# Optimization experiments

Hardware: AMD Instinct MI355X
Metric: run time of the kernel (lower is better)

Reference implementation:

```python
import jax, jax.numpy as jnp
import numpy as np

N = 50000
E = 600000
D = 128
H = 8
DH = D // H
SCALE = float(np.sqrt(DH))


def setup_inputs() -> dict:
    key = jax.random.key(0)
    ks = jax.random.split(key, 12)
    s = 1.0 / np.sqrt(D)
    return {
        "x": jax.random.normal(ks[0], (N, D), jnp.float32),
        "edge_index": jax.random.randint(ks[1], (2, E), 0, N, jnp.int64),
        "edge_attr": jax.random.normal(ks[2], (E,), jnp.float32),
        "Wq": jax.random.uniform(ks[3], (D, D), jnp.float32, -s, s),
        "bq": jax.random.uniform(ks[4], (D,), jnp.float32, -s, s),
        "Wk": jax.random.uniform(ks[5], (D, D), jnp.float32, -s, s),
        "bk": jax.random.uniform(ks[6], (D,), jnp.float32, -s, s),
        "Wv": jax.random.uniform(ks[7], (D, D), jnp.float32, -s, s),
        "bv": jax.random.uniform(ks[8], (D,), jnp.float32, -s, s),
        "Wo": jax.random.uniform(ks[9], (D, D), jnp.float32, -s, s),
        "bo": jax.random.uniform(ks[10], (D,), jnp.float32, -s, s),
    }


def reference(x, edge_index, edge_attr, Wq, bq, Wk, bk, Wv, bv, Wo, bo):
    # Projections -> [N, H, DH]
    Q = (x @ Wq + bq).reshape(N, H, DH)
    K = (x @ Wk + bk).reshape(N, H, DH)
    V = (x @ Wv + bv).reshape(N, H, DH)
    row, col = edge_index[0], edge_index[1]
    q_i = Q[row]   # [E, H, DH] gather by destination (source of softmax segment)
    k_j = K[col]
    v_j = V[col]
    scores = jnp.sum(q_i * k_j, axis=-1) / SCALE  # [E, H]
    scores = scores + edge_attr[:, None]          # edge_attr broadcast over heads
    # Segment softmax per row-node; max is taken over heads then per node (as original)
    edge_max = scores.max(axis=1)                                  # [E]
    node_max = jax.ops.segment_max(edge_max, row, num_segments=N)  # [N]
    s_exp = jnp.exp(scores - node_max[row][:, None])               # [E, H]
    s_sum = jax.ops.segment_sum(s_exp, row, num_segments=N)        # [N, H]
    attn = s_exp / (s_sum[row] + 1e-8)                             # [E, H]
    # (dropout is identity in eval mode)
    out = jax.ops.segment_sum(attn[:, :, None] * v_j, row, num_segments=N)  # [N, H, DH]
    out = out.reshape(N, D)
    return out @ Wo + bo
```

## Files before the change

kernel.cpp:

```cpp
#include <hip/hip_runtime.h>
#include <math.h>

#define N_NODES 50000
#define N_EDGES 600000
#define DIM 128
#define HEADS 8
#define EBLK 2344
#define GBLK 1563
#define NB1 586
#define L1E 1024

typedef _Float16 v8h __attribute__((ext_vector_type(8)));
typedef _Float16 v2h __attribute__((ext_vector_type(2)));
typedef float v16f __attribute__((ext_vector_type(16)));
typedef float v2f __attribute__((ext_vector_type(2)));

union v8h_u {
    v8h v;
    v2h p[4];
    _Float16 e[8];
};

__device__ __forceinline__ float e4m3_to_f32_sw(unsigned int b) {
    unsigned int s = b >> 7, E = (b >> 3) & 0xF, m = b & 7;
    float v = (E == 0) ? (float)m * 0.001953125f
                       : ldexpf(1.0f + (float)m * 0.125f, (int)E - 7);
    return s ? -v : v;
}

template <bool HI>
__device__ __forceinline__ v2f cvt2_f8(unsigned int w) {
#if __has_builtin(__builtin_amdgcn_cvt_pk_f32_fp8)
    return __builtin_amdgcn_cvt_pk_f32_fp8((int)w, HI);
#else
    v2f r;
    r[0] = e4m3_to_f32_sw((w >> (HI ? 16 : 0)) & 0xff);
    r[1] = e4m3_to_f32_sw((w >> (HI ? 24 : 8)) & 0xff);
    return r;
#endif
}

__device__ __forceinline__ unsigned char f32_to_e4m3(float v) {
#if __has_builtin(__builtin_amdgcn_cvt_pk_fp8_f32)
    return (unsigned char)(__builtin_amdgcn_cvt_pk_fp8_f32(v, v, 0, false) & 0xff);
#else
    float a = fabsf(v);
    unsigned char sgn = (v < 0.f) ? 0x80 : 0;
    if (!(a >= 0.0078125f)) {
        int m = (int)(a * 512.0f + 0.5f);
        if (m > 7) return sgn | 8;
        return sgn | (unsigned char)m;
    }
    if (a >= 448.0f) return sgn | 0x7e;
    int e;
    float fr = frexpf(a, &e);
    int mant = (int)(fr * 16.0f + 0.5f);
    int E = e + 6;
    if (mant == 16) { mant = 8; E++; }
    if (E >= 16) return sgn | 0x7e;
    return sgn | (unsigned char)((E << 3) | (mant - 8));
#endif
}

__global__ __launch_bounds__(256) void prep_kernel(const float* __restrict__ Wq,
                                                   const float* __restrict__ Wk,
                                                   const float* __restrict__ Wv,
                                                   const float* __restrict__ Wo,
                                                   _Float16* __restrict__ Wfrag) {
    int i = blockIdx.x * 256 + threadIdx.x;
    if (i < 16384) {
        int base = i * 4;
        int mat = i >> 12;
        int rem = i & 4095;
        int wave = rem >> 10;
        int kt = (rem >> 7) & 7;
        int lane = (rem >> 1) & 63;
        int jh = (rem & 1) * 4;
        const float* src = (mat == 0) ? Wq : (mat == 1) ? Wk : (mat == 2) ? Wv : Wo;
        int n = wave * 32 + (lane & 31);
        int kbase = kt * 16 + (lane >> 5) * 8 + jh;
        _Float16 o[4];
#pragma unroll
        for (int j = 0; j < 4; j++) o[j] = (_Float16)src[(kbase + j) * 128 + n];
        *(short4*)(Wfrag + base) = *(short4*)o;
    }
}

#define LDSTRIDE 132
__global__ __launch_bounds__(256) void qkv_hist(const float* __restrict__ x,
                                                const _Float16* __restrict__ Wfrag,
                                                const float* __restrict__ bq,
                                                const float* __restrict__ bk,
                                                const float* __restrict__ bv,
                                                _Float16* __restrict__ Qh,
                                                unsigned char* __restrict__ K8,
                                                _Float16* __restrict__ Vh,
                                                const int* __restrict__ rowi,
                                                int* __restrict__ bh) {
    __shared__ _Float16 As[32 * LDSTRIDE];
    __shared__ int lh[256];
    if (blockIdx.x >= GBLK) {
        int b = blockIdx.x - GBLK;
        int t = threadIdx.x;
        lh[t] = 0;
        __syncthreads();
        int e0 = b * L1E + t;
#pragma unroll
        for (int k = 0; k < 4; k++) {
            int e = e0 + k * 256;
            if (e < N_EDGES) atomicAdd(lh + (rowi[e] >> 8), 1);
        }
        __syncthreads();
        bh[t * NB1 + b] = lh[t];
        return;
    }
    int tid = threadIdx.x;
    int wave = tid >> 6, lane = tid & 63;
    int m32 = lane & 31, quad = lane >> 5;
    int row0 = blockIdx.x * 32;

    {
        int r = tid >> 3;
        int c0 = (tid & 7) * 16;
        int gr = row0 + r;
        bool valid = gr < N_NODES;
        const float4* src = (const float4*)(x + (size_t)gr * 128 + c0);
        _Float16* dst = As + r * LDSTRIDE + c0;
#pragma unroll
        for (int q = 0; q < 4; q++) {
            float4 v = valid ? src[q] : make_float4(0.f, 0.f, 0.f, 0.f);
            _Float16 o[4] = {(_Float16)v.x, (_Float16)v.y, (_Float16)v.z, (_Float16)v.w};
            *(short4*)(dst + q * 4) = *(short4*)o;
        }
    }
    __syncthreads();

    v8h af[8];
#pragma unroll
    for (int kt = 0; kt < 8; kt++)
        af[kt] = *(const v8h*)(As + m32 * LDSTRIDE + kt * 16 + quad * 8);

    int col = wave * 32 + m32;
#pragma unroll
    for (int mat = 0; mat < 3; mat++) {
        const _Float16* wf = Wfrag + mat * 16384 + wave * 4096 + lane * 8;
        v16f acc;
#pragma unroll
        for (int r = 0; r < 16; r++) acc[r] = 0.0f;
#pragma unroll
        for (int kt = 0; kt < 8; kt++) {
            v8h bf = *(const v8h*)(wf + kt * 512);
            acc = __builtin_amdgcn_mfma_f32_32x32x16_f16(af[kt], bf, acc, 0, 0, 0);
        }
        const float* bias = (mat == 0) ? bq : (mat == 1) ? bk : bv;
        float bias_v = bias[col];
        if (mat == 1) {
#pragma unroll
            for (int r = 0; r < 16; r++) {
                int row = (r & 3) + 8 * (r >> 2) + 4 * quad;
                int gr = row0 + row;
                if (gr < N_NODES) K8[(size_t)gr * 128 + col] = f32_to_e4m3(acc[r] + bias_v);
            }
        } else {
            _Float16* C = (mat == 0) ? Qh : Vh;
#pragma unroll
            for (int r = 0; r < 16; r++) {
                int row = (r & 3) + 8 * (r >> 2) + 4 * quad;
                int gr = row0 + row;
                if (gr < N_NODES) C[(size_t)gr * 128 + col] = (_Float16)(acc[r] + bias_v);
            }
        }
    }
}

__global__ __launch_bounds__(256) void scanA(const int* __restrict__ bh,
                                             int* __restrict__ within,
                                             int* __restrict__ dt) {
    __shared__ int sh[256];
    int d = blockIdx.x, t = threadIdx.x;
    int carry = 0;
    for (int c = 0; c < 3; c++) {
        int j = c * 256 + t;
        int v = (j < NB1) ? bh[d * NB1 + j] : 0;
        __syncthreads();
        sh[t] = v;
        __syncthreads();
        for (int off = 1; off < 256; off <<= 1) {
            int a = sh[t];
            int b2 = (t >= off) ? sh[t - off] : 0;
            __syncthreads();
            sh[t] = a + b2;
            __syncthreads();
        }
        if (j < NB1) within[d * NB1 + j] = carry + sh[t] - v;
        carry += sh[255];
    }
    if (t == 0) dt[d] = carry;
}

__global__ __launch_bounds__(256) void scanB(const int* __restrict__ dt,
                                             int* __restrict__ dto) {
    __shared__ int sh[256];
    int t = threadIdx.x;
    int v = dt[t];
    sh[t] = v;
    __syncthreads();
    for (int off = 1; off < 256; off <<= 1) {
        int a = sh[t];
        int b2 = (t >= off) ? sh[t - off] : 0;
        __syncthreads();
        sh[t] = a + b2;
        __syncthreads();
    }
    dto[t] = sh[t] - v;
}

__global__ __launch_bounds__(256) void l1scat(const int* __restrict__ rowi,
                                              const int* __restrict__ coli,
                                              const float* __restrict__ eattr,
                                              const int* __restrict__ within,
                                              const int* __restrict__ dto,
                                              unsigned long long* __restrict__ rec1) {
    __shared__ int lh[256], base[256];
    int b = blockIdx.x, t = threadIdx.x;
    lh[t] = 0;
    base[t] = dto[t] + within[t * NB1 + b];
    __syncthreads();
    int e0 = b * L1E + t;
#pragma unroll
    for (int k = 0; k < 4; k++) {
        int e = e0 + k * 256;
        if (e < N_EDGES) {
            int row = rowi[e];
            int d = row >> 8;
            int r = atomicAdd(lh + d, 1);
            unsigned short eb = __builtin_bit_cast(unsigned short, (_Float16)eattr[e]);
            rec1[base[d] + r] = (unsigned long long)row |
                                ((unsigned long long)(unsigned int)coli[e] << 16) |
                                ((unsigned long long)eb << 32);
        }
    }
}

__global__ __launch_bounds__(256) void l2sort(const unsigned long long* __restrict__ rec1,
                                              const int* __restrict__ dto,
                                              const int* __restrict__ dt,
                                              int* __restrict__ counts,
                                              int* __restrict__ start,
                                              unsigned int* __restrict__ ep4) {
    __shared__ int h[256], hs[256], r2[256], sh[256];
    int d = blockIdx.x, t = threadIdx.x;
    int s = dto[d], cnt = dt[d];
    int e = s + cnt;
    h[t] = 0;
    r2[t] = 0;
    __syncthreads();
    for (int i = s + t; i < e; i += 256) atomicAdd(h + (int)(rec1[i] & 255), 1);
    __syncthreads();
    int v = h[t];
    sh[t] = v;
    __syncthreads();
    for (int off = 1; off < 256; off <<= 1) {
        int a = sh[t];
        int b2 = (t >= off) ? sh[t - off] : 0;
        __syncthreads();
        sh[t] = a + b2;
        __syncthreads();
    }
    int ex = sh[t] - v;
    hs[t] = ex;
    int node = (d << 8) | t;
    if (node < N_NODES) {
        counts[node] = v;
        start[node] = s + ex;
    }
    __syncthreads();
    for (int i = s + t; i < e; i += 256) {
        unsigned long long w = rec1[i];
        int ld = (int)(w & 255);
        int r = atomicAdd(r2 + ld, 1);
        ep4[s + hs[ld] + r] = (unsigned int)(w >> 16);
    }
}

__global__ __launch_bounds__(256) void gemm_out(const _Float16* __restrict__ Ah,
                                                const _Float16* __restrict__ Wfrag,
                                                const float* __restrict__ bo,
                                                float* __restrict__ C) {
    __shared__ _Float16 As[32 * LDSTRIDE];
    int tid = threadIdx.x;
    int wave = tid >> 6, lane = tid & 63;
    int m32 = lane & 31, quad = lane >> 5;
    int row0 = blockIdx.x * 32;

    {
        int r = tid >> 3;
        int c0 = (tid & 7) * 16;
        int gr = row0 + r;
        bool valid = gr < N_NODES;
        const v8h* src = (const v8h*)(Ah + (size_t)gr * 128 + c0);
        _Float16* dst = As + r * LDSTRIDE + c0;
        v8h z = {};
        *(v8h*)(dst) = valid ? src[0] : z;
        *(v8h*)(dst + 8) = valid ? src[1] : z;
    }
    __syncthreads();

    v8h af[8];
#pragma unroll
    for (int kt = 0; kt < 8; kt++)
        af[kt] = *(const v8h*)(As + m32 * LDSTRIDE + kt * 16 + quad * 8);

    int col = wave * 32 + m32;
    const _Float16* wf = Wfrag + 3 * 16384 + wave * 4096 + lane * 8;
    v16f acc;
#pragma unroll
    for (int r = 0; r < 16; r++) acc[r] = 0.0f;
#pragma unroll
    for (int kt = 0; kt < 8; kt++) {
        v8h bf = *(const v8h*)(wf + kt * 512);
        acc = __builtin_amdgcn_mfma_f32_32x32x16_f16(af[kt], bf, acc, 0, 0, 0);
    }
    float bias_v = bo[col];
#pragma unroll
    for (int r = 0; r < 16; r++) {
        int row = (r & 3) + 8 * (r >> 2) + 4 * quad;
        int gr = row0 + row;
        if (gr < N_NODES) C[(size_t)gr * 128 + col] = acc[r] + bias_v;
    }
}

__global__ __launch_bounds__(256) void fused_attn(const _Float16* __restrict__ Q,
                                                  const unsigned char* __restrict__ K8,
                                                  const _Float16* __restrict__ V,
                                                  const int* __restrict__ start,
                                                  const int* __restrict__ counts,
                                                  const unsigned int* __restrict__ ep4,
                                                  _Float16* __restrict__ Aout) {
    int t = blockIdx.x * 256 + threadIdx.x;
    int n = t >> 4;
    int sub = t & 15;
    if (n >= N_NODES) return;

    int s0 = start[n];
    int cnt = counts[n];
    int e1 = s0 + cnt;

    v8h_u q;
    q.v = *(const v8h*)(Q + (size_t)n * 128 + sub * 8);
    float qf[8];
#pragma unroll
    for (int j = 0; j < 8; j++) qf[j] = (float)q.e[j];

    const unsigned char* Kb = K8 + sub * 8;
    const _Float16* Vb = V + sub * 8;

    float l = 0.0f;
    float acc[8];
#pragma unroll
    for (int j = 0; j < 8; j++) acc[j] = 0.0f;

    int nb = (cnt + 15) >> 4;
    for (int b = 0; b < nb; b++) {
        int base = s0 + (b << 4);
        int li = base + sub;
        if (li >= e1) li = e1 - 1;
        unsigned int pv = ep4[li];

#pragma unroll
        for (int h = 0; h < 2; h++) {
            int hb = h << 3;
            if (base + hb < e1) {
                int cols[8];
                float eas[8];
#pragma unroll
                for (int u = 0; u < 8; u++) {
                    unsigned int w = (unsigned int)__shfl((int)pv, hb + u, 16);
                    cols[u] = (int)(w & 0xffffu);
                    eas[u] = (float)__builtin_bit_cast(_Float16, (unsigned short)(w >> 16));
                }
                uint2 kw[8];
                v8h_u vv[8];
#pragma unroll
                for (int u = 0; u < 8; u++) {
                    kw[u] = *(const uint2*)(Kb + ((size_t)cols[u] << 7));
                    vv[u].v = *(const v8h*)(Vb + ((size_t)cols[u] << 7));
                }
                __builtin_amdgcn_sched_barrier(0);
#pragma unroll
                for (int u = 0; u < 8; u++) {
                    v2f k01 = cvt2_f8<false>(kw[u].x);
                    v2f k23 = cvt2_f8<true>(kw[u].x);
                    v2f k45 = cvt2_f8<false>(kw[u].y);
                    v2f k67 = cvt2_f8<true>(kw[u].y);
                    float dot = 0.0f;
                    dot = fmaf(qf[0], k01[0], dot);
                    dot = fmaf(qf[1], k01[1], dot);
                    dot = fmaf(qf[2], k23[0], dot);
                    dot = fmaf(qf[3], k23[1], dot);
                    dot = fmaf(qf[4], k45[0], dot);
                    dot = fmaf(qf[5], k45[1], dot);
                    dot = fmaf(qf[6], k67[0], dot);
                    dot = fmaf(qf[7], k67[1], dot);
                    dot += __shfl_xor(dot, 1);
                    float s = dot * 0.25f + eas[u];
                    bool valid = (base + hb + u) < e1;
                    float ex = valid ? __expf(s) : 0.0f;
                    l += ex;
#pragma unroll
                    for (int j = 0; j < 8; j++) acc[j] = fmaf(ex, (float)vv[u].e[j], acc[j]);
                }
            }
        }
    }

    float inv = 1.0f / (l + 1e-8f);
    _Float16 tmp[8];
#pragma unroll
    for (int j = 0; j < 8; j++) tmp[j] = (_Float16)(acc[j] * inv);
    *(v8h*)(Aout + (size_t)n * 128 + sub * 8) = *(v8h*)tmp;
}

extern "C" void kernel_launch(void* const* d_in, const int* in_sizes, int n_in,
                              void* d_out, int out_size, void* d_ws, size_t ws_size,
                              hipStream_t stream) {
    const float* x = (const float*)d_in[0];
    const int* ei = (const int*)d_in[1];
    const float* eattr = (const float*)d_in[2];
    const float* Wq = (const float*)d_in[3];
    const float* bq = (const float*)d_in[4];
    const float* Wk = (const float*)d_in[5];
    const float* bk = (const float*)d_in[6];
    const float* Wv = (const float*)d_in[7];
    const float* bv = (const float*)d_in[8];
    const float* Wo = (const float*)d_in[9];
    const float* bo = (const float*)d_in[10];
    float* out = (float*)d_out;

    const int* rowi = ei;
    const int* coli = ei + N_EDGES;

    _Float16* Qh = (_Float16*)d_ws;
    _Float16* Vh = Qh + (size_t)N_NODES * DIM;
    _Float16* Ah = Vh + (size_t)N_NODES * DIM;
    unsigned char* K8 = (unsigned char*)(Ah + (size_t)N_NODES * DIM);
    _Float16* Wfrag = (_Float16*)(K8 + (size_t)N_NODES * DIM);
    int* counts = (int*)(Wfrag + 4 * 16384);
    int* start = counts + N_NODES;
    int* bh = start + N_NODES;
    int* within = bh + 256 * NB1;
    int* dt = within + 256 * NB1;
    int* dto = dt + 256;
    unsigned long long* rec1 = (unsigned long long*)(dto + 256);
    unsigned int* ep4 = (unsigned int*)(rec1 + N_EDGES);

    prep_kernel<<<64, 256, 0, stream>>>(Wq, Wk, Wv, Wo, Wfrag);
    qkv_hist<<<GBLK + NB1, 256, 0, stream>>>(x, Wfrag, bq, bk, bv, Qh, K8, Vh,
                                             rowi, bh);
    scanA<<<256, 256, 0, stream>>>(bh, within, dt);
    scanB<<<1, 256, 0, stream>>>(dt, dto);
    l1scat<<<NB1, 256, 0, stream>>>(rowi, coli, eattr, within, dto, rec1);
    l2sort<<<196, 256, 0, stream>>>(rec1, dto, dt, counts, start, ep4);
    int ablocks = (N_NODES * 16 + 255) / 256;
    fused_attn<<<ablocks, 256, 0, stream>>>(Qh, K8, Vh, start, counts, ep4, Ah);
    gemm_out<<<GBLK, 256, 0, stream>>>(Ah, Wfrag, bo, out);
}
```

Measured before the change: 177.0 us.

## Merge sort pipeline stages into fewer launches using cooperative grid sync

Moves the row histogram into the weight-prep kernel and the per-digit scan into the QKV GEMM kernel. Each block now recomputes the small digit-total scan redundantly, and the level-1 scatter and level-2 sort run in one cooperative kernel separated by a grid sync. Together this cuts the launch count from eight to five, removing launch gaps and the serial single-block scan. The cost is a grid-wide barrier, a dependence on all 586 blocks being co-resident for the cooperative launch, and scan work repeated in every block.

New measurement: 261.5 us. 1.48x slower.

```diff
diff --git a/kernel.cpp b/kernel.cpp
--- a/kernel.cpp
+++ b/kernel.cpp
@@ -1,11 +1,13 @@
 #include <hip/hip_runtime.h>
+#include <hip/hip_cooperative_groups.h>
 #include <math.h>
+
+namespace cg = cooperative_groups;
 
 #define N_NODES 50000
 #define N_EDGES 600000
 #define DIM 128
 #define HEADS 8
-#define EBLK 2344
 #define GBLK 1563
 #define NB1 586
 #define L1E 1024
@@ -62,32 +64,48 @@
 #endif
 }
 
-__global__ __launch_bounds__(256) void prep_kernel(const float* __restrict__ Wq,
-                                                   const float* __restrict__ Wk,
-                                                   const float* __restrict__ Wv,
-                                                   const float* __restrict__ Wo,
-                                                   _Float16* __restrict__ Wfrag) {
+__global__ __launch_bounds__(256) void prep_hist(const float* __restrict__ Wq,
+                                                 const float* __restrict__ Wk,
+                                                 const float* __restrict__ Wv,
+                                                 const float* __restrict__ Wo,
+                                                 _Float16* __restrict__ Wfrag,
+                                                 const int* __restrict__ rowi,
+                                                 int* __restrict__ bh) {
+    __shared__ int lh[256];
+    if (blockIdx.x >= 64) {
+        int b = blockIdx.x - 64;
+        int t = threadIdx.x;
+        lh[t] = 0;
+        __syncthreads();
+        int e0 = b * L1E + t;
+#pragma unroll
+        for (int k = 0; k < 4; k++) {
+            int e = e0 + k * 256;
+            if (e < N_EDGES) atomicAdd(lh + (rowi[e] >> 8), 1);
+        }
+        __syncthreads();
+        bh[t * NB1 + b] = lh[t];
+        return;
+    }
     int i = blockIdx.x * 256 + threadIdx.x;
-    if (i < 16384) {
-        int base = i * 4;
-        int mat = i >> 12;
-        int rem = i & 4095;
-        int wave = rem >> 10;
-        int kt = (rem >> 7) & 7;
-        int lane = (rem >> 1) & 63;
-        int jh = (rem & 1) * 4;
-        const float* src = (mat == 0) ? Wq : (mat == 1) ? Wk : (mat == 2) ? Wv : Wo;
-        int n = wave * 32 + (lane & 31);
-        int kbase = kt * 16 + (lane >> 5) * 8 + jh;
-        _Float16 o[4];
-#pragma unroll
-        for (int j = 0; j < 4; j++) o[j] = (_Float16)src[(kbase + j) * 128 + n];
-        *(short4*)(Wfrag + base) = *(short4*)o;
-    }
+    int base = i * 4;
+    int mat = i >> 12;
+    int rem = i & 4095;
+    int wave = rem >> 10;
+    int kt = (rem >> 7) & 7;
+    int lane = (rem >> 1) & 63;
+    int jh = (rem & 1) * 4;
+    const float* src = (mat == 0) ? Wq : (mat == 1) ? Wk : (mat == 2) ? Wv : Wo;
+    int n = wave * 32 + (lane & 31);
+    int kbase = kt * 16 + (lane >> 5) * 8 + jh;
+    _Float16 o[4];
+#pragma unroll
+    for (int j = 0; j < 4; j++) o[j] = (_Float16)src[(kbase + j) * 128 + n];
+    *(short4*)(Wfrag + base) = *(short4*)o;
 }
 
 #define LDSTRIDE 132
-__global__ __launch_bounds__(256) void qkv_hist(const float* __restrict__ x,
+__global__ __launch_bounds__(256) void qkv_scan(const float* __restrict__ x,
                                                 const _Float16* __restrict__ Wfrag,
                                                 const float* __restrict__ bq,
                                                 const float* __restrict__ bk,
@@ -95,23 +113,32 @@
                                                 _Float16* __restrict__ Qh,
                                                 unsigned char* __restrict__ K8,
                                                 _Float16* __restrict__ Vh,
-                                                const int* __restrict__ rowi,
-                                                int* __restrict__ bh) {
+                                                const int* __restrict__ bh,
+                                                int* __restrict__ within,
+                                                int* __restrict__ dt) {
     __shared__ _Float16 As[32 * LDSTRIDE];
-    __shared__ int lh[256];
+    __shared__ int sh[256];
     if (blockIdx.x >= GBLK) {
-        int b = blockIdx.x - GBLK;
+        int d = blockIdx.x - GBLK;
         int t = threadIdx.x;
-        lh[t] = 0;
-        __syncthreads();
-        int e0 = b * L1E + t;
-#pragma unroll
-        for (int k = 0; k < 4; k++) {
-            int e = e0 + k * 256;
-            if (e < N_EDGES) atomicAdd(lh + (rowi[e] >> 8), 1);
-        }
-        __syncthreads();
-        bh[t * NB1 + b] = lh[t];
+        int carry = 0;
+        for (int c = 0; c < 3; c++) {
+            int j = c * 256 + t;
+            int v = (j < NB1) ? bh[d * NB1 + j] : 0;
+            __syncthreads();
+            sh[t] = v;
+            __syncthreads();
+            for (int off = 1; off < 256; off <<= 1) {
+                int a = sh[t];
+                int b2 = (t >= off) ? sh[t - off] : 0;
+                __syncthreads();
+                sh[t] = a + b2;
+                __syncthreads();
+            }
+            if (j < NB1) within[d * NB1 + j] = carry + sh[t] - v;
+            carry += sh[255];
+        }
+        if (t == 0) dt[d] = carry;
         return;
     }
     int tid = threadIdx.x;
@@ -173,58 +200,33 @@
     }
 }
 
-__global__ __launch_bounds__(256) void scanA(const int* __restrict__ bh,
-                                             int* __restrict__ within,
-                                             int* __restrict__ dt) {
-    __shared__ int sh[256];
-    int d = blockIdx.x, t = threadIdx.x;
-    int carry = 0;
-    for (int c = 0; c < 3; c++) {
-        int j = c * 256 + t;
-        int v = (j < NB1) ? bh[d * NB1 + j] : 0;
-        __syncthreads();
-        sh[t] = v;
-        __syncthreads();
-        for (int off = 1; off < 256; off <<= 1) {
-            int a = sh[t];
-            int b2 = (t >= off) ? sh[t - off] : 0;
-            __syncthreads();
-            sh[t] = a + b2;
-            __syncthreads();
-        }
-        if (j < NB1) within[d * NB1 + j] = carry + sh[t] - v;
-        carry += sh[255];
-    }
-    if (t == 0) dt[d] = carry;
-}
-
-__global__ __launch_bounds__(256) void scanB(const int* __restrict__ dt,
-                                             int* __restrict__ dto) {
-    __shared__ int sh[256];
-    int t = threadIdx.x;
+__global__ __launch_bounds__(256) void sortk(const int* __restrict__ rowi,
+                                             const int* __restrict__ coli,
+                                             const float* __restrict__ eattr,
+                                             const int* __restrict__ within,
+                                             const int* __restrict__ dt,
+                                             unsigned long long* __restrict__ rec1,
+                                             int* __restrict__ counts,
+                                             int* __restrict__ start,
+                                             unsigned int* __restrict__ ep4) {
+    cg::grid_group grid = cg::this_grid();
+    __shared__ int s0_[256], s1_[256], s2_[256], s3_[256];
+    int b = blockIdx.x, t = threadIdx.x;
+
     int v = dt[t];
-    sh[t] = v;
+    s0_[t] = v;
     __syncthreads();
     for (int off = 1; off < 256; off <<= 1) {
-        int a = sh[t];
-        int b2 = (t >= off) ? sh[t - off] : 0;
-        __syncthreads();
-        sh[t] = a + b2;
-        __syncthreads();
-    }
-    dto[t] = sh[t] - v;
-}
-
-__global__ __launch_bounds__(256) void l1scat(const int* __restrict__ rowi,
-                                              const int* __restrict__ coli,
-                                              const float* __restrict__ eattr,
-                                              const int* __restrict__ within,
-                                              const int* __restrict__ dto,
-                                              unsigned long long* __restrict__ rec1) {
-    __shared__ int lh[256], base[256];
-    int b = blockIdx.x, t = threadIdx.x;
-    lh[t] = 0;
-    base[t] = dto[t] + within[t * NB1 + b];
+        int a = s0_[t];
+        int b2 = (t >= off) ? s0_[t - off] : 0;
+        __syncthreads();
+        s0_[t] = a + b2;
+        __syncthreads();
+    }
+    s3_[t] = s0_[t] - v;
+
+    s1_[t] = 0;
+    s2_[t] = s3_[t] + within[t * NB1 + b];
     __syncthreads();
     int e0 = b * L1E + t;
 #pragma unroll
@@ -233,53 +235,51 @@
         if (e < N_EDGES) {
             int row = rowi[e];
             int d = row >> 8;
-            int r = atomicAdd(lh + d, 1);
+            int r = atomicAdd(s1_ + d, 1);
             unsigned short eb = __builtin_bit_cast(unsigned short, (_Float16)eattr[e]);
-            rec1[base[d] + r] = (unsigned long long)row |
-                                ((unsigned long long)(unsigned int)coli[e] << 16) |
-                                ((unsigned long long)eb << 32);
-        }
-    }
-}
-
-__global__ __launch_bounds__(256) void l2sort(const unsigned long long* __restrict__ rec1,
-                                              const int* __restrict__ dto,
-                                              const int* __restrict__ dt,
-                                              int* __restrict__ counts,
-                                              int* __restrict__ start,
-                                              unsigned int* __restrict__ ep4) {
-    __shared__ int h[256], hs[256], r2[256], sh[256];
-    int d = blockIdx.x, t = threadIdx.x;
-    int s = dto[d], cnt = dt[d];
-    int e = s + cnt;
-    h[t] = 0;
-    r2[t] = 0;
-    __syncthreads();
-    for (int i = s + t; i < e; i += 256) atomicAdd(h + (int)(rec1[i] & 255), 1);
-    __syncthreads();
-    int v = h[t];
-    sh[t] = v;
-    __syncthreads();
-    for (int off = 1; off < 256; off <<= 1) {
-        int a = sh[t];
-        int b2 = (t >= off) ? sh[t - off] : 0;
-        __syncthreads();
-        sh[t] = a + b2;
-        __syncthreads();
-    }
-    int ex = sh[t] - v;
-    hs[t] = ex;
-    int node = (d << 8) | t;
-    if (node < N_NODES) {
-        counts[node] = v;
-        start[node] = s + ex;
-    }
-    __syncthreads();
-    for (int i = s + t; i < e; i += 256) {
-        unsigned long long w = rec1[i];
-        int ld = (int)(w & 255);
-        int r = atomicAdd(r2 + ld, 1);
-        ep4[s + hs[ld] + r] = (unsigned int)(w >> 16);
+            rec1[s2_[d] + r] = (unsigned long long)row |
+                               ((unsigned long long)(unsigned int)coli[e] << 16) |
+                               ((unsigned long long)eb << 32);
+        }
+    }
+
+    grid.sync();
+
+    if (b < 196) {
+        int d = b;
+        int seg = s3_[d];
+        int cnt = dt[d];
+        int e = seg + cnt;
+        __syncthreads();
+        s0_[t] = 0;
+        s2_[t] = 0;
+        __syncthreads();
+        for (int i = seg + t; i < e; i += 256) atomicAdd(s0_ + (int)(rec1[i] & 255), 1);
+        __syncthreads();
+        int hv = s0_[t];
+        s3_[t] = hv;
+        __syncthreads();
+        for (int off = 1; off < 256; off <<= 1) {
+            int a = s3_[t];
+            int b2 = (t >= off) ? s3_[t - off] : 0;
+            __syncthreads();
+            s3_[t] = a + b2;
+            __syncthreads();
+        }
+        int ex = s3_[t] - hv;
+        s1_[t] = ex;
+        int node = (d << 8) | t;
+        if (node < N_NODES) {
+            counts[node] = hv;
+            start[node] = seg + ex;
+        }
+        __syncthreads();
+        for (int i = seg + t; i < e; i += 256) {
+            unsigned long long w = rec1[i];
+            int ld = (int)(w & 255);
+            int r = atomicAdd(s2_ + ld, 1);
+            ep4[seg + s1_[ld] + r] = (unsigned int)(w >> 16);
+        }
     }
 }
 
@@ -450,17 +450,26 @@
     int* bh = start + N_NODES;
     int* within = bh + 256 * NB1;
     int* dt = within + 256 * NB1;
-    int* dto = dt + 256;
-    unsigned long long* rec1 = (unsigned long long*)(dto + 256);
+    unsigned long long* rec1 = (unsigned long long*)(dt + 256);
     unsigned int* ep4 = (unsigned int*)(rec1 + N_EDGES);
 
-    prep_kernel<<<64, 256, 0, stream>>>(Wq, Wk, Wv, Wo, Wfrag);
-    qkv_hist<<<GBLK + NB1, 256, 0, stream>>>(x, Wfrag, bq, bk, bv, Qh, K8, Vh,
-                                             rowi, bh);
-    scanA<<<256, 256, 0, stream>>>(bh, within, dt);
-    scanB<<<1, 256, 0, stream>>>(dt, dto);
-    l1scat<<<NB1, 256, 0, stream>>>(rowi, coli, eattr, within, dto, rec1);
-    l2sort<<<196, 256, 0, stream>>>(rec1, dto, dt, counts, start, ep4);
+    prep_hist<<<64 + NB1, 256, 0, stream>>>(Wq, Wk, Wv, Wo, Wfrag, rowi, bh);
+    qkv_scan<<<GBLK + 256, 256, 0, stream>>>(x, Wfrag, bq, bk, bv, Qh, K8, Vh,
+                                             bh, within, dt);
+    {
+        void* rowi_p = (void*)rowi;
+        void* coli_p = (void*)coli;
+        void* eattr_p = (void*)eattr;
+        void* within_p = (void*)within;
+        void* dt_p = (void*)dt;
+        void* rec1_p = (void*)rec1;
+        void* counts_p = (void*)counts;
+        void* start_p = (void*)start;
+        void* ep4_p = (void*)ep4;
+        void* args[] = {&rowi_p, &coli_p, &eattr_p, &within_p, &dt_p,
+                        &rec1_p, &counts_p, &start_p, &ep4_p};
+        hipLaunchCooperativeKernel((void*)sortk, dim3(NB1), dim3(256), args, 0, stream);
+    }
     int ablocks = (N_NODES * 16 + 255) / 256;
     fused_attn<<<ablocks, 256, 0, stream>>>(Qh, K8, Vh, start, counts, ep4, Ah);
     gemm_out<<<GBLK, 256, 0, stream>>>(Ah, Wfrag, bo, out);
```

## Merge histogram into prep, scan into QKV GEMM, recompute scanB inline

Applied to the files above, without the earlier changes.

Moves the per-block row histogram into the weight-prep launch and the per-bucket scan into the QKV GEMM launch as extra blocks. The single-block exclusive scan over bucket totals is dropped and recomputed redundantly inside every l1scat and l2sort block. This cuts the pipeline from eight launches to six, removing launch gaps and serial tiny kernels, at the cost of redundant scan work per block.

Result: no change. 177.7 us (+0.4%).

```diff
diff --git a/kernel.cpp b/kernel.cpp
--- a/kernel.cpp
+++ b/kernel.cpp
@@ -5,7 +5,6 @@
 #define N_EDGES 600000
 #define DIM 128
 #define HEADS 8
-#define EBLK 2344
 #define GBLK 1563
 #define NB1 586
 #define L1E 1024
@@ -62,32 +61,48 @@
 #endif
 }
 
-__global__ __launch_bounds__(256) void prep_kernel(const float* __restrict__ Wq,
-                                                   const float* __restrict__ Wk,
-                                                   const float* __restrict__ Wv,
-                                                   const float* __restrict__ Wo,
-                                                   _Float16* __restrict__ Wfrag) {
+__global__ __launch_bounds__(256) void prep_hist(const float* __restrict__ Wq,
+                                                 const float* __restrict__ Wk,
+                                                 const float* __restrict__ Wv,
+                                                 const float* __restrict__ Wo,
+                                                 _Float16* __restrict__ Wfrag,
+                                                 const int* __restrict__ rowi,
+                                                 int* __restrict__ bh) {
+    __shared__ int lh[256];
+    if (blockIdx.x >= 64) {
+        int b = blockIdx.x - 64;
+        int t = threadIdx.x;
+        lh[t] = 0;
+        __syncthreads();
+        int e0 = b * L1E + t;
+#pragma unroll
+        for (int k = 0; k < 4; k++) {
+            int e = e0 + k * 256;
+            if (e < N_EDGES) atomicAdd(lh + (rowi[e] >> 8), 1);
+        }
+        __syncthreads();
+        bh[t * NB1 + b] = lh[t];
+        return;
+    }
     int i = blockIdx.x * 256 + threadIdx.x;
-    if (i < 16384) {
-        int base = i * 4;
-        int mat = i >> 12;
-        int rem = i & 4095;
-        int wave = rem >> 10;
-        int kt = (rem >> 7) & 7;
-        int lane = (rem >> 1) & 63;
-        int jh = (rem & 1) * 4;
-        const float* src = (mat == 0) ? Wq : (mat == 1) ? Wk : (mat == 2) ? Wv : Wo;
-        int n = wave * 32 + (lane & 31);
-        int kbase = kt * 16 + (lane >> 5) * 8 + jh;
-        _Float16 o[4];
-#pragma unroll
-        for (int j = 0; j < 4; j++) o[j] = (_Float16)src[(kbase + j) * 128 + n];
-        *(short4*)(Wfrag + base) = *(short4*)o;
-    }
+    int base = i * 4;
+    int mat = i >> 12;
+    int rem = i & 4095;
+    int wave = rem >> 10;
+    int kt = (rem >> 7) & 7;
+    int lane = (rem >> 1) & 63;
+    int jh = (rem & 1) * 4;
+    const float* src = (mat == 0) ? Wq : (mat == 1) ? Wk : (mat == 2) ? Wv : Wo;
+    int n = wave * 32 + (lane & 31);
+    int kbase = kt * 16 + (lane >> 5) * 8 + jh;
+    _Float16 o[4];
+#pragma unroll
+    for (int j = 0; j < 4; j++) o[j] = (_Float16)src[(kbase + j) * 128 + n];
+    *(short4*)(Wfrag + base) = *(short4*)o;
 }
 
 #define LDSTRIDE 132
-__global__ __launch_bounds__(256) void qkv_hist(const float* __restrict__ x,
+__global__ __launch_bounds__(256) void qkv_scan(const float* __restrict__ x,
                                                 const _Float16* __restrict__ Wfrag,
                                                 const float* __restrict__ bq,
                                                 const float* __restrict__ bk,
@@ -95,23 +110,32 @@
                                                 _Float16* __restrict__ Qh,
                                                 unsigned char* __restrict__ K8,
                                                 _Float16* __restrict__ Vh,
-                                                const int* __restrict__ rowi,
-                                                int* __restrict__ bh) {
+                                                const int* __restrict__ bh,
+                                                int* __restrict__ within,
+                                                int* __restrict__ dt) {
     __shared__ _Float16 As[32 * LDSTRIDE];
-    __shared__ int lh[256];
+    __shared__ int sh[256];
     if (blockIdx.x >= GBLK) {
-        int b = blockIdx.x - GBLK;
+        int d = blockIdx.x - GBLK;
         int t = threadIdx.x;
-        lh[t] = 0;
-        __syncthreads();
-        int e0 = b * L1E + t;
-#pragma unroll
-        for (int k = 0; k < 4; k++) {
-            int e = e0 + k * 256;
-            if (e < N_EDGES) atomicAdd(lh + (rowi[e] >> 8), 1);
-        }
-        __syncthreads();
-        bh[t * NB1 + b] = lh[t];
+        int carry = 0;
+        for (int c = 0; c < 3; c++) {
+            int j = c * 256 + t;
+            int v = (j < NB1) ? bh[d * NB1 + j] : 0;
+            __syncthreads();
+            sh[t] = v;
+            __syncthreads();
+            for (int off = 1; off < 256; off <<= 1) {
+                int a = sh[t];
+                int b2 = (t >= off) ? sh[t - off] : 0;
+                __syncthreads();
+                sh[t] = a + b2;
+                __syncthreads();
+            }
+            if (j < NB1) within[d * NB1 + j] = carry + sh[t] - v;
+            carry += sh[255];
+        }
+        if (t == 0) dt[d] = carry;
         return;
     }
     int tid = threadIdx.x;
@@ -173,58 +197,27 @@
     }
 }
 
-__global__ __launch_bounds__(256) void scanA(const int* __restrict__ bh,
-                                             int* __restrict__ within,
-                                             int* __restrict__ dt) {
-    __shared__ int sh[256];
-    int d = blockIdx.x, t = threadIdx.x;
-    int carry = 0;
-    for (int c = 0; c < 3; c++) {
-        int j = c * 256 + t;
-        int v = (j < NB1) ? bh[d * NB1 + j] : 0;
-        __syncthreads();
-        sh[t] = v;
-        __syncthreads();
-        for (int off = 1; off < 256; off <<= 1) {
-            int a = sh[t];
-            int b2 = (t >= off) ? sh[t - off] : 0;
-            __syncthreads();
-            sh[t] = a + b2;
-            __syncthreads();
-        }
-        if (j < NB1) within[d * NB1 + j] = carry + sh[t] - v;
-        carry += sh[255];
-    }
-    if (t == 0) dt[d] = carry;
-}
-
-__global__ __launch_bounds__(256) void scanB(const int* __restrict__ dt,
-                                             int* __restrict__ dto) {
-    __shared__ int sh[256];
-    int t = threadIdx.x;
-    int v = dt[t];
-    sh[t] = v;
-    __syncthreads();
-    for (int off = 1; off < 256; off <<= 1) {
-        int a = sh[t];
-        int b2 = (t >= off) ? sh[t - off] : 0;
-        __syncthreads();
-        sh[t] = a + b2;
-        __syncthreads();
-    }
-    dto[t] = sh[t] - v;
-}
-
 __global__ __launch_bounds__(256) void l1scat(const int* __restrict__ rowi,
                                               const int* __restrict__ coli,
                                               const float* __restrict__ eattr,
                                               const int* __restrict__ within,
-                                              const int* __restrict__ dto,
+                                              const int* __restrict__ dt,
                                               unsigned long long* __restrict__ rec1) {
-    __shared__ int lh[256], base[256];
+    __shared__ int lh[256], base[256], sh[256];
     int b = blockIdx.x, t = threadIdx.x;
+    int v = dt[t];
+    sh[t] = v;
+    __syncthreads();
+    for (int off = 1; off < 256; off <<= 1) {
+        int a = sh[t];
+        int b2 = (t >= off) ? sh[t - off] : 0;
+        __syncthreads();
+        sh[t] = a + b2;
+        __syncthreads();
+    }
+    int dto = sh[t] - v;
     lh[t] = 0;
-    base[t] = dto[t] + within[t * NB1 + b];
+    base[t] = dto + within[t * NB1 + b];
     __syncthreads();
     int e0 = b * L1E + t;
 #pragma unroll
@@ -243,15 +236,26 @@
 }
 
 __global__ __launch_bounds__(256) void l2sort(const unsigned long long* __restrict__ rec1,
-                                              const int* __restrict__ dto,
                                               const int* __restrict__ dt,
                                               int* __restrict__ counts,
                                               int* __restrict__ start,
                                               unsigned int* __restrict__ ep4) {
     __shared__ int h[256], hs[256], r2[256], sh[256];
     int d = blockIdx.x, t = threadIdx.x;
-    int s = dto[d], cnt = dt[d];
+    int v0 = dt[t];
+    sh[t] = v0;
+    __syncthreads();
+    for (int off = 1; off < 256; off <<= 1) {
+        int a = sh[t];
+        int b2 = (t >= off) ? sh[t - off] : 0;
+        __syncthreads();
+        sh[t] = a + b2;
+        __syncthreads();
+    }
+    int cnt = dt[d];
+    int s = sh[d] - cnt;
     int e = s + cnt;
+    __syncthreads();
     h[t] = 0;
     r2[t] = 0;
     __syncthreads();
@@ -450,17 +454,14 @@
     int* bh = start + N_NODES;
     int* within = bh + 256 * NB1;
     int* dt = within + 256 * NB1;
-    int* dto = dt + 256;
-    unsigned long long* rec1 = (unsigned long long*)(dto + 256);
+    unsigned long long* rec1 = (unsigned long long*)(dt + 256);
     unsigned int* ep4 = (unsigned int*)(rec1 + N_EDGES);
 
-    prep_kernel<<<64, 256, 0, stream>>>(Wq, Wk, Wv, Wo, Wfrag);
-    qkv_hist<<<GBLK + NB1, 256, 0, stream>>>(x, Wfrag, bq, bk, bv, Qh, K8, Vh,
-                                             rowi, bh);
-    scanA<<<256, 256, 0, stream>>>(bh, within, dt);
-    scanB<<<1, 256, 0, stream>>>(dt, dto);
-    l1scat<<<NB1, 256, 0, stream>>>(rowi, coli, eattr, within, dto, rec1);
-    l2sort<<<196, 256, 0, stream>>>(rec1, dto, dt, counts, start, ep4);
+    prep_hist<<<64 + NB1, 256, 0, stream>>>(Wq, Wk, Wv, Wo, Wfrag, rowi, bh);
+    qkv_scan<<<GBLK + 256, 256, 0, stream>>>(x, Wfrag, bq, bk, bv, Qh, K8, Vh,
+                                             bh, within, dt);
+    l1scat<<<NB1, 256, 0, stream>>>(rowi, coli, eattr, within, dt, rec1);
+    l2sort<<<196, 256, 0, stream>>>(rec1, dt, counts, start, ep4);
     int ablocks = (N_NODES * 16 + 255) / 256;
     fused_attn<<<ablocks, 256, 0, stream>>>(Qh, K8, Vh, start, counts, ep4, Ah);
     gemm_out<<<GBLK, 256, 0, stream>>>(Ah, Wfrag, bo, out);
```
